# Performance work log

Measured on AMD Instinct MI355X. Metric: run time of the kernel, lower is better.

Reference implementation:

```python
import jax, jax.numpy as jnp
import numpy as np

EMBED_DIM = 1024
NUM_HEADS = 16
HEAD_DIM = EMBED_DIM // NUM_HEADS
SEQ_LEN = 2048
BATCH = 2


def setup_inputs() -> dict:
    key = jax.random.key(0)
    ks = jax.random.split(key, 9)
    s = 1.0 / np.sqrt(EMBED_DIM)
    inputs = jax.random.normal(ks[0], (BATCH, SEQ_LEN, EMBED_DIM), dtype=jnp.float32)
    Wq = jax.random.uniform(ks[1], (EMBED_DIM, EMBED_DIM), jnp.float32, -s, s)
    bq = jax.random.uniform(ks[2], (EMBED_DIM,), jnp.float32, -s, s)
    Wk = jax.random.uniform(ks[3], (EMBED_DIM, EMBED_DIM), jnp.float32, -s, s)
    bk = jax.random.uniform(ks[4], (EMBED_DIM,), jnp.float32, -s, s)
    Wv = jax.random.uniform(ks[5], (EMBED_DIM, EMBED_DIM), jnp.float32, -s, s)
    bv = jax.random.uniform(ks[6], (EMBED_DIM,), jnp.float32, -s, s)
    Wo = jax.random.uniform(ks[7], (EMBED_DIM, EMBED_DIM), jnp.float32, -s, s)
    bo = jax.random.uniform(ks[8], (EMBED_DIM,), jnp.float32, -s, s)
    return {"inputs": inputs, "Wq": Wq, "bq": bq, "Wk": Wk, "bk": bk,
            "Wv": Wv, "bv": bv, "Wo": Wo, "bo": bo}


def reference(inputs, Wq, bq, Wk, bk, Wv, bv, Wo, bo):
    B, S, D = inputs.shape
    H, Hd = NUM_HEADS, HEAD_DIM

    def heads(x):  # [B,S,D] -> [B,H,S,Hd]
        return x.reshape(B, S, H, Hd).transpose(0, 2, 1, 3)

    q = heads(inputs @ Wq + bq)
    k = heads(inputs @ Wk + bk)
    v = heads(inputs @ Wv + bv)

    # [B,H,S,S] causal scores (naive, matching original module)
    scores = jnp.einsum('bhqd,bhkd->bhqk', q, k) * (Hd ** -0.5)
    causal = jnp.tril(jnp.ones((S, S), dtype=bool))
    scores = jnp.where(causal, scores, jnp.float32(-jnp.inf))
    attn = jax.nn.softmax(scores, axis=-1)

    out = jnp.einsum('bhqk,bhkd->bhqd', attn, v)
    out = out.transpose(0, 2, 1, 3).reshape(B, S, D)
    return out @ Wo + bo
```

## Files before the change

kernel.cpp:

```cpp
#include <hip/hip_runtime.h>
#include <stdint.h>
#include <stddef.h>

#define SEQ   2048
#define DIM   1024
#define NH    16
#define HD    64
#define MTOT  4096
#define LPAD  72
#define EPAD  136
#define FPAD  132
#define QSCALE 0.18033688f

typedef __attribute__((ext_vector_type(8))) short short8;
typedef __attribute__((ext_vector_type(4))) float floatx4;
typedef __attribute__((ext_vector_type(16))) float floatx16;
typedef __attribute__((ext_vector_type(4))) float float4v;
typedef __attribute__((ext_vector_type(4))) unsigned short ushort4v;
typedef __attribute__((ext_vector_type(4))) unsigned int uint4v;

__device__ __forceinline__ floatx4 mfma_bf16(short8 a, short8 b, floatx4 c) {
    return __builtin_amdgcn_mfma_f32_16x16x32_bf16(a, b, c, 0, 0, 0);
}
__device__ __forceinline__ floatx16 mfma32(short8 a, short8 b, floatx16 c) {
    return __builtin_amdgcn_mfma_f32_32x32x16_bf16(a, b, c, 0, 0, 0);
}

__device__ __forceinline__ float b2f(unsigned short s) {
    unsigned int u = ((unsigned int)s) << 16;
    return __builtin_bit_cast(float, u);
}
__device__ __forceinline__ unsigned short f2b(float f) {
    unsigned int u = __builtin_bit_cast(unsigned int, f);
    u += 0x7fffu + ((u >> 16) & 1u);
    return (unsigned short)(u >> 16);
}
__device__ __forceinline__ unsigned int cvtpk(float lo, float hi) {
    unsigned int w;
    asm("v_cvt_pk_bf16_f32 %0, %1, %2" : "=v"(w) : "v"(lo), "v"(hi));
    return w;
}
__device__ __forceinline__ void swap32(unsigned int& a, unsigned int& b) {
    asm("v_permlane32_swap_b32 %0, %1" : "+v"(a), "+v"(b));
}
__device__ __forceinline__ float exp2v(float x) {
    float r;
    asm("v_exp_f32 %0, %1" : "=v"(r) : "v"(x));
    return r;
}
__device__ __forceinline__ short8 mk8(unsigned int a, unsigned int b,
                                      unsigned int c, unsigned int d) {
    uint4v u; u.x = a; u.y = b; u.z = c; u.w = d;
    return __builtin_bit_cast(short8, u);
}
__device__ __forceinline__ void g2l16(const unsigned short* g, unsigned short* l) {
    __builtin_amdgcn_global_load_lds(
        (const __attribute__((address_space(1))) void*)g,
        (__attribute__((address_space(3))) void*)l, 16, 0, 0);
}

__global__ __launch_bounds__(256) void prep_all(const float* __restrict__ w0,
                                                const float* __restrict__ w1,
                                                const float* __restrict__ w2,
                                                const float* __restrict__ w3,
                                                unsigned short* __restrict__ outbase,
                                                const float* __restrict__ xin,
                                                unsigned short* __restrict__ xout) {
    const int z = blockIdx.z;
    const int tid = threadIdx.x;
    if (z >= 4) {
        const int cblk = (z - 4) * 256 + blockIdx.y * 16 + blockIdx.x;
        const int i = (cblk * 256 + tid) * 4;
        const float4v v = *(const float4v*)&xin[i];
        ushort4v o;
        o.x = f2b(v.x); o.y = f2b(v.y); o.z = f2b(v.z); o.w = f2b(v.w);
        *(ushort4v*)&xout[i] = o;
        return;
    }
    __shared__ float t[64][65];
    const float* in = (z == 0) ? w0 : (z == 1) ? w1 : (z == 2) ? w2 : w3;
    unsigned short* out = outbase + (size_t)z * DIM * DIM;
    const int c0 = blockIdx.x * 64, r0 = blockIdx.y * 64;
    const int x = tid & 63, y = tid >> 6;
#pragma unroll
    for (int i = 0; i < 64; i += 4)
        t[y + i][x] = in[(size_t)(r0 + y + i) * DIM + c0 + x];
    __syncthreads();
#pragma unroll
    for (int i = 0; i < 64; i += 4)
        out[(size_t)(c0 + y + i) * DIM + r0 + x] = f2b(t[x][y + i]);
}

__global__ __launch_bounds__(256) void gemm_fused(const unsigned short* __restrict__ A,
                                                  const unsigned short* __restrict__ WTbase,
                                                  const float* __restrict__ b0,
                                                  const float* __restrict__ b1,
                                                  const float* __restrict__ b2,
                                                  void* __restrict__ outbase,
                                                  int qkv) {
    __shared__ __attribute__((aligned(16))) unsigned short smem[2 * 128 * LPAD];
    unsigned short* As = smem;
    unsigned short* Bs = smem + 128 * 64;

    const int z = blockIdx.z;
    const unsigned short* BT = WTbase + (size_t)z * (DIM * DIM);
    const float* bias        = (z == 0) ? b0 : (z == 1) ? b1 : b2;
    const int mode = qkv ? ((z == 0) ? 1 : (z == 1) ? 3 : 4) : 0;
    float* Cf          = (float*)outbase;
    unsigned short* Cb = (unsigned short*)outbase + (size_t)z * ((size_t)MTOT * DIM);

    const int tid = threadIdx.x;
    const int w = tid >> 6, lane = tid & 63;
    const int quad = lane >> 4, l16 = lane & 15;
    const int wm = w >> 1, wn = w & 1;
    const int m0 = blockIdx.x * 128, n0 = blockIdx.y * 128;
    const int bb = m0 >> 11;

    floatx4 acc[4][4];
#pragma unroll
    for (int mi = 0; mi < 4; ++mi)
#pragma unroll
        for (int ni = 0; ni < 4; ++ni) acc[mi][ni] = (floatx4)0.0f;

    const int srow8 = lane >> 3;
    const int sgs8  = ((lane & 7) ^ srow8) * 8;
    const unsigned short* gA = &A [(size_t)(m0 + w * 8 + srow8) * DIM + sgs8];
    const unsigned short* gB = &BT[(size_t)(n0 + w * 8 + srow8) * DIM + sgs8];

    const int sx = l16 & 7;

    for (int k0 = 0; ; k0 += 64) {
#pragma unroll
        for (int i = 0; i < 4; ++i) {
            g2l16(gA + (size_t)i * (32 * DIM) + k0, &As[(i * 4 + w) * 512]);
            g2l16(gB + (size_t)i * (32 * DIM) + k0, &Bs[(i * 4 + w) * 512]);
        }
        __syncthreads();
#pragma unroll
        for (int kk = 0; kk < 2; ++kk) {
            short8 a[4], b[4];
#pragma unroll
            for (int mi = 0; mi < 4; ++mi)
                a[mi] = *(const short8*)&As[(wm * 64 + mi * 16 + l16) * 64 +
                                            (((kk * 4) + quad) ^ sx) * 8];
#pragma unroll
            for (int ni = 0; ni < 4; ++ni)
                b[ni] = *(const short8*)&Bs[(wn * 64 + ni * 16 + l16) * 64 +
                                            (((kk * 4) + quad) ^ sx) * 8];
#pragma unroll
            for (int mi = 0; mi < 4; ++mi)
#pragma unroll
                for (int ni = 0; ni < 4; ++ni)
                    acc[mi][ni] = mfma_bf16(a[mi], b[ni], acc[mi][ni]);
        }
        if (k0 + 64 >= DIM) break;
        __syncthreads();
    }

    float bvv[4];
#pragma unroll
    for (int ni = 0; ni < 4; ++ni) bvv[ni] = bias[n0 + wn * 64 + ni * 16 + l16];

    if (mode == 0) {
        float* T = (float*)smem;
        for (int p = 0; p < 4; ++p) {
            __syncthreads();
            if (wm == (p >> 1)) {
                const int mib = (p & 1) * 2;
#pragma unroll
                for (int mm = 0; mm < 2; ++mm)
#pragma unroll
                    for (int ni = 0; ni < 4; ++ni)
#pragma unroll
                        for (int r = 0; r < 4; ++r)
                            T[(mm * 16 + quad * 4 + r) * FPAD + wn * 64 + ni * 16 + l16] =
                                acc[mib + mm][ni][r] + bvv[ni];
            }
            __syncthreads();
#pragma unroll
            for (int it = 0; it < 4; ++it) {
                const int c = it * 256 + tid;
                const int row = c >> 5, nof = (c & 31) * 4;
                *(float4v*)&Cf[(size_t)(m0 + p * 32 + row) * DIM + n0 + nof] =
                    *(const float4v*)&T[row * FPAD + nof];
            }
        }
    } else if (mode == 1) {
        unsigned short* T = smem;
        __syncthreads();
#pragma unroll
        for (int mi = 0; mi < 4; ++mi)
#pragma unroll
            for (int ni = 0; ni < 4; ++ni)
#pragma unroll
                for (int r = 0; r < 4; ++r)
                    T[(wm * 64 + mi * 16 + quad * 4 + r) * EPAD + wn * 64 + ni * 16 + l16] =
                        f2b((acc[mi][ni][r] + bvv[ni]) * QSCALE);
        __syncthreads();
#pragma unroll
        for (int it = 0; it < 8; ++it) {
            const int c = it * 256 + tid;
            const int seg = c >> 3, d8 = (c & 7) * 8;
            const int mm = seg >> 1, hseg = seg & 1;
            const int h = (n0 >> 6) + hseg;
            const int s = (m0 & (SEQ - 1)) + mm;
            *(short8*)&Cb[((size_t)(bb * NH + h) * SEQ + s) * HD + d8] =
                *(const short8*)&T[mm * EPAD + hseg * 64 + d8];
        }
    } else if (mode == 3) {
        unsigned short* T = smem;
        __syncthreads();
#pragma unroll
        for (int mi = 0; mi < 4; ++mi)
#pragma unroll
            for (int ni = 0; ni < 4; ++ni)
#pragma unroll
                for (int r = 0; r < 4; ++r)
                    T[(wm * 64 + mi * 16 + quad * 4 + r) * EPAD + wn * 64 + ni * 16 + l16] =
                        f2b(acc[mi][ni][r] + bvv[ni]);
        __syncthreads();
#pragma unroll
        for (int it = 0; it < 8; ++it) {
            const int f = it * 256 + tid;
            const int ln = f & 63, fragid = f >> 6;
            const int h2 = fragid >> 4;
            const int jb = (fragid >> 2) & 3;
            const int c  = fragid & 3;
            const short8 v = *(const short8*)&T[(jb * 32 + (ln & 31)) * EPAD +
                                                h2 * 64 + c * 16 + (ln >> 5) * 8];
            const int bh = bb * NH + (n0 >> 6) + h2;
            const int jg = ((m0 & (SEQ - 1)) >> 5) + jb;
            *(short8*)&Cb[(((size_t)bh * 64 + jg) * 4 + c) * 512 + ln * 8] = v;
        }
    } else {
        unsigned short* T = smem;
        __syncthreads();
#pragma unroll
        for (int mi = 0; mi < 4; ++mi)
#pragma unroll
            for (int ni = 0; ni < 4; ++ni) {
                ushort4v pk;
#pragma unroll
                for (int r = 0; r < 4; ++r) pk[r] = f2b(acc[mi][ni][r] + bvv[ni]);
                *(ushort4v*)&T[(wn * 64 + ni * 16 + l16) * EPAD + wm * 64 + mi * 16 + quad * 4] = pk;
            }
        __syncthreads();
#pragma unroll
        for (int it = 0; it < 8; ++it) {
            const int f = it * 256 + tid;
            const int ln = f & 63, fragid = f >> 6;
            const int h2 = fragid >> 4;
            const int jb = (fragid >> 2) & 3;
            const int dk = fragid & 3;
            const int d0 = dk >> 1, kk = dk & 1;
            const short8 v = *(const short8*)&T[(h2 * 64 + d0 * 32 + (ln & 31)) * EPAD +
                                                jb * 32 + kk * 16 + (ln >> 5) * 8];
            const int bh = bb * NH + (n0 >> 6) + h2;
            const int jg = ((m0 & (SEQ - 1)) >> 5) + jb;
            *(short8*)&Cb[(((size_t)bh * 64 + jg) * 4 + dk) * 512 + ln * 8] = v;
        }
    }
}

__global__ __launch_bounds__(256) void attn_fwd(const unsigned short* __restrict__ Q,
                                                const unsigned short* __restrict__ KP,
                                                const unsigned short* __restrict__ VP,
                                                unsigned short* __restrict__ O) {
    __shared__ float Fo[4][32][68];
    __shared__ float Fl[4][32];

    const int bh = blockIdx.x;
    const int pr = blockIdx.y;
    const int tid = threadIdx.x;
    const int w = tid >> 6, lane = tid & 63;
    const int ql  = lane & 31;
    const int hi  = lane >> 5;
    const int hi4 = hi * 4;
    const int hi8 = hi * 8;

    const unsigned short* Qh  = Q  + (size_t)bh * SEQ * HD;
    const unsigned short* KPh = KP + (size_t)bh * (64 * 2048);
    const unsigned short* VPh = VP + (size_t)bh * (64 * 2048);
    const int bb = bh >> 4, h = bh & 15;

#define LOADKV(KF, VF) do {                                                  \
        _Pragma("unroll")                                                    \
        for (int c_ = 0; c_ < 4; ++c_) {                                     \
            KF[c_] = *(const short8*)(kp + c_ * 512);                        \
            VF[c_] = *(const short8*)(vp + c_ * 512);                        \
        }                                                                    \
        kp += 4 * 2048; vp += 4 * 2048;                                      \
    } while (0)

#define ATT_BLOCK(KF, VF, MASKED) do {                                       \
        floatx16 st_ = (floatx16)0.0f;                                       \
        __builtin_amdgcn_s_setprio(1);                                       \
        _Pragma("unroll")                                                    \
        for (int c_ = 0; c_ < 4; ++c_) st_ = mfma32(KF[c_], qf[c_], st_);    \
        __builtin_amdgcn_s_setprio(0);                                       \
        float p_[16];                                                        \
        _Pragma("unroll")                                                    \
        for (int r_ = 0; r_ < 16; ++r_) {                                    \
            float e_ = exp2v(st_[r_]);                                       \
            if (MASKED)                                                      \
                e_ = (((r_ & 3) + 8 * (r_ >> 2) + hi4) > ql) ? 0.0f : e_;    \
            p_[r_] = e_;                                                     \
        }                                                                    \
        l0 += (p_[0] + p_[1]) + (p_[2] + p_[3]);                             \
        l1 += (p_[4] + p_[5]) + (p_[6] + p_[7]);                             \
        l0 += (p_[8] + p_[9]) + (p_[10] + p_[11]);                           \
        l1 += (p_[12] + p_[13]) + (p_[14] + p_[15]);                         \
        unsigned int w0_ = cvtpk(p_[0], p_[1]),   w2_ = cvtpk(p_[4], p_[5]); \
        unsigned int w1_ = cvtpk(p_[2], p_[3]),   w3_ = cvtpk(p_[6], p_[7]); \
        unsigned int w4_ = cvtpk(p_[8], p_[9]),   w6_ = cvtpk(p_[12], p_[13]); \
        unsigned int w5_ = cvtpk(p_[10], p_[11]), w7_ = cvtpk(p_[14], p_[15]); \
        swap32(w0_, w2_); swap32(w1_, w3_);                                  \
        swap32(w4_, w6_); swap32(w5_, w7_);                                  \
        const short8 pa0_ = mk8(w0_, w1_, w2_, w3_);                         \
        const short8 pa1_ = mk8(w4_, w5_, w6_, w7_);                         \
        __builtin_amdgcn_s_setprio(1);                                       \
        o_acc0 = mfma32(pa0_, VF[0], o_acc0);                                \
        o_acc1 = mfma32(pa0_, VF[2], o_acc1);                                \
        o_acc0 = mfma32(pa1_, VF[1], o_acc0);                                \
        o_acc1 = mfma32(pa1_, VF[3], o_acc1);                                \
        __builtin_amdgcn_s_setprio(0);                                       \
    } while (0)

#pragma unroll 1
    for (int t = 0; t < 2; ++t) {
        const int qc = t ? pr : (63 - pr);
        const int q0 = qc * 32;

        short8 qf[4];
#pragma unroll
        for (int c = 0; c < 4; ++c)
            qf[c] = *(const short8*)(Qh + (size_t)(q0 + ql) * HD + c * 16 + hi8);

        floatx16 o_acc0 = (floatx16)0.0f, o_acc1 = (floatx16)0.0f;
        float l0 = 0.0f, l1 = 0.0f;

        const int n = (qc >= w) ? ((qc - w) >> 2) + 1 : 0;
        const bool lastmask = ((qc & 3) == w);
        const unsigned short* kp = KPh + (size_t)w * 2048 + lane * 8;
        const unsigned short* vp = VPh + (size_t)w * 2048 + lane * 8;

        if (n > 0) {
            short8 kfA[4], vfA[4], kfB[4], vfB[4];
            LOADKV(kfA, vfA);
            int b = 0;
            while (b + 2 <= n - 1) {
                LOADKV(kfB, vfB);
                ATT_BLOCK(kfA, vfA, 0);
                LOADKV(kfA, vfA);
                ATT_BLOCK(kfB, vfB, 0);
                b += 2;
            }
            if (b == n - 2) {
                LOADKV(kfB, vfB);
                ATT_BLOCK(kfA, vfA, 0);
                ATT_BLOCK(kfB, vfB, lastmask);
            } else {
                ATT_BLOCK(kfA, vfA, lastmask);
            }
        }

        float* Fow = &Fo[w][0][0];
#pragma unroll
        for (int r = 0; r < 16; ++r) {
            const int row = (r & 3) + 8 * (r >> 2) + hi4;
            Fow[row * 68 + ql]      = o_acc0[r];
            Fow[row * 68 + 32 + ql] = o_acc1[r];
        }
        float l = l0 + l1;
        l += __shfl_xor(l, 32, 64);
        if (lane < 32) Fl[w][lane] = l;
        __syncthreads();

        const int rrow = w * 8 + (lane >> 3);
        const int c8   = (lane & 7) * 8;
        float s[8];
#pragma unroll
        for (int e = 0; e < 8; ++e) s[e] = 0.0f;
#pragma unroll
        for (int ww = 0; ww < 4; ++ww) {
            const float* src = &Fo[ww][rrow][c8];
            const float4v a = *(const float4v*)&src[0];
            const float4v b2 = *(const float4v*)&src[4];
            s[0] += a.x;  s[1] += a.y;  s[2] += a.z;  s[3] += a.w;
            s[4] += b2.x; s[5] += b2.y; s[6] += b2.z; s[7] += b2.w;
        }
        const float lt = (Fl[0][rrow] + Fl[1][rrow]) + (Fl[2][rrow] + Fl[3][rrow]);
        const float iv = 1.0f / lt;
        const unsigned int o0 = cvtpk(s[0] * iv, s[1] * iv);
        const unsigned int o1 = cvtpk(s[2] * iv, s[3] * iv);
        const unsigned int o2 = cvtpk(s[4] * iv, s[5] * iv);
        const unsigned int o3 = cvtpk(s[6] * iv, s[7] * iv);
        *(short8*)&O[(size_t)(bb * SEQ + q0 + rrow) * DIM + h * HD + c8] =
            mk8(o0, o1, o2, o3);
        __syncthreads();
    }
#undef LOADKV
#undef ATT_BLOCK
}

extern "C" void kernel_launch(void* const* d_in, const int* in_sizes, int n_in,
                              void* d_out, int out_size, void* d_ws, size_t ws_size,
                              hipStream_t stream) {
    const float* X  = (const float*)d_in[0];
    const float* Wq = (const float*)d_in[1];
    const float* bq = (const float*)d_in[2];
    const float* Wk = (const float*)d_in[3];
    const float* bk = (const float*)d_in[4];
    const float* Wv = (const float*)d_in[5];
    const float* bv = (const float*)d_in[6];
    const float* Wo = (const float*)d_in[7];
    const float* bo = (const float*)d_in[8];

    unsigned short* ws = (unsigned short*)d_ws;
    const size_t WSZ = (size_t)DIM * DIM;
    const size_t TSZ = (size_t)MTOT * DIM;
    unsigned short* WqT = ws;
    unsigned short* WoT = ws + 3 * WSZ;
    unsigned short* Qb  = ws + 4 * WSZ;
    unsigned short* Kp  = Qb + TSZ;
    unsigned short* Vp  = Kp + TSZ;
    unsigned short* Ob  = Vp + TSZ;

    unsigned short* Xb = (unsigned short*)d_out;

    prep_all<<<dim3(16, 16, 20), 256, 0, stream>>>(Wq, Wk, Wv, Wo, WqT, X, Xb);

    gemm_fused<<<dim3(MTOT / 128, DIM / 128, 3), 256, 0, stream>>>(
        Xb, WqT, bq, bk, bv, (void*)Qb, 1);

    attn_fwd<<<dim3(2 * NH, 32), 256, 0, stream>>>(Qb, Kp, Vp, Ob);

    gemm_fused<<<dim3(MTOT / 128, DIM / 128, 1), 256, 0, stream>>>(
        Ob, WoT, bo, bo, bo, d_out, 0);
}
```

Baseline: 171.9 us.

## Use single-wave attention blocks per query tile instead of 4-wave KV split

The attention kernel now launches one 64-thread wave per 32-row query tile, and that wave walks the whole causal KV range itself. Previously four waves split the KV blocks and reduced partial outputs through shared memory, and each block handled two paired query tiles for load balance. This drops the cross-wave float reduction and its barriers, and launches more, smaller blocks ordered heaviest-first. In exchange, each wave has a longer serial dependency chain, and balance now relies on the hardware scheduler. The row-sum accumulation was also moved after the PV MFMAs to overlap with them.

```diff
diff --git a/kernel.cpp b/kernel.cpp
--- a/kernel.cpp
+++ b/kernel.cpp
@@ -262,17 +262,16 @@
     }
 }
 
-__global__ __launch_bounds__(256) void attn_fwd(const unsigned short* __restrict__ Q,
-                                                const unsigned short* __restrict__ KP,
-                                                const unsigned short* __restrict__ VP,
-                                                unsigned short* __restrict__ O) {
-    __shared__ float Fo[4][32][68];
-    __shared__ float Fl[4][32];
+__global__ __launch_bounds__(64) void attn_fwd(const unsigned short* __restrict__ Q,
+                                               const unsigned short* __restrict__ KP,
+                                               const unsigned short* __restrict__ VP,
+                                               unsigned short* __restrict__ O) {
+    __shared__ __attribute__((aligned(16))) unsigned short Os[32 * LPAD];
+    __shared__ float Linv[32];
 
     const int bh = blockIdx.x;
-    const int pr = blockIdx.y;
-    const int tid = threadIdx.x;
-    const int w = tid >> 6, lane = tid & 63;
+    const int qc = (gridDim.y - 1) - blockIdx.y;
+    const int lane = threadIdx.x;
     const int ql  = lane & 31;
     const int hi  = lane >> 5;
     const int hi4 = hi * 4;
@@ -281,7 +280,18 @@
     const unsigned short* Qh  = Q  + (size_t)bh * SEQ * HD;
     const unsigned short* KPh = KP + (size_t)bh * (64 * 2048);
     const unsigned short* VPh = VP + (size_t)bh * (64 * 2048);
-    const int bb = bh >> 4, h = bh & 15;
+    const int q0 = qc * 32;
+
+    short8 qf[4];
+#pragma unroll
+    for (int c = 0; c < 4; ++c)
+        qf[c] = *(const short8*)(Qh + (size_t)(q0 + ql) * HD + c * 16 + hi8);
+
+    floatx16 o_acc0 = (floatx16)0.0f, o_acc1 = (floatx16)0.0f;
+    float l0 = 0.0f, l1 = 0.0f;
+
+    const unsigned short* kp = KPh + lane * 8;
+    const unsigned short* vp = VPh + lane * 8;
 
 #define LOADKV(KF, VF) do {                                                  \
         _Pragma("unroll")                                                    \
@@ -289,7 +299,7 @@
             KF[c_] = *(const short8*)(kp + c_ * 512);                        \
             VF[c_] = *(const short8*)(vp + c_ * 512);                        \
         }                                                                    \
-        kp += 4 * 2048; vp += 4 * 2048;                                      \
+        kp += 2048; vp += 2048;                                              \
     } while (0)
 
 #define ATT_BLOCK(KF, VF, MASKED) do {                                       \
@@ -306,10 +316,6 @@
                 e_ = (((r_ & 3) + 8 * (r_ >> 2) + hi4) > ql) ? 0.0f : e_;    \
             p_[r_] = e_;                                                     \
         }                                                                    \
-        l0 += (p_[0] + p_[1]) + (p_[2] + p_[3]);                             \
-        l1 += (p_[4] + p_[5]) + (p_[6] + p_[7]);                             \
-        l0 += (p_[8] + p_[9]) + (p_[10] + p_[11]);                           \
-        l1 += (p_[12] + p_[13]) + (p_[14] + p_[15]);                         \
         unsigned int w0_ = cvtpk(p_[0], p_[1]),   w2_ = cvtpk(p_[4], p_[5]); \
         unsigned int w1_ = cvtpk(p_[2], p_[3]),   w3_ = cvtpk(p_[6], p_[7]); \
         unsigned int w4_ = cvtpk(p_[8], p_[9]),   w6_ = cvtpk(p_[12], p_[13]); \
@@ -324,80 +330,50 @@
         o_acc0 = mfma32(pa1_, VF[1], o_acc0);                                \
         o_acc1 = mfma32(pa1_, VF[3], o_acc1);                                \
         __builtin_amdgcn_s_setprio(0);                                       \
+        l0 += (p_[0] + p_[1]) + (p_[2] + p_[3]);                             \
+        l1 += (p_[4] + p_[5]) + (p_[6] + p_[7]);                             \
+        l0 += (p_[8] + p_[9]) + (p_[10] + p_[11]);                           \
+        l1 += (p_[12] + p_[13]) + (p_[14] + p_[15]);                         \
     } while (0)
 
-#pragma unroll 1
-    for (int t = 0; t < 2; ++t) {
-        const int qc = t ? pr : (63 - pr);
-        const int q0 = qc * 32;
-
-        short8 qf[4];
-#pragma unroll
-        for (int c = 0; c < 4; ++c)
-            qf[c] = *(const short8*)(Qh + (size_t)(q0 + ql) * HD + c * 16 + hi8);
-
-        floatx16 o_acc0 = (floatx16)0.0f, o_acc1 = (floatx16)0.0f;
-        float l0 = 0.0f, l1 = 0.0f;
-
-        const int n = (qc >= w) ? ((qc - w) >> 2) + 1 : 0;
-        const bool lastmask = ((qc & 3) == w);
-        const unsigned short* kp = KPh + (size_t)w * 2048 + lane * 8;
-        const unsigned short* vp = VPh + (size_t)w * 2048 + lane * 8;
-
-        if (n > 0) {
-            short8 kfA[4], vfA[4], kfB[4], vfB[4];
-            LOADKV(kfA, vfA);
-            int b = 0;
-            while (b + 2 <= n - 1) {
-                LOADKV(kfB, vfB);
-                ATT_BLOCK(kfA, vfA, 0);
-                LOADKV(kfA, vfA);
-                ATT_BLOCK(kfB, vfB, 0);
-                b += 2;
-            }
-            if (b == n - 2) {
-                LOADKV(kfB, vfB);
-                ATT_BLOCK(kfA, vfA, 0);
-                ATT_BLOCK(kfB, vfB, lastmask);
-            } else {
-                ATT_BLOCK(kfA, vfA, lastmask);
-            }
-        }
-
-        float* Fow = &Fo[w][0][0];
-#pragma unroll
-        for (int r = 0; r < 16; ++r) {
-            const int row = (r & 3) + 8 * (r >> 2) + hi4;
-            Fow[row * 68 + ql]      = o_acc0[r];
-            Fow[row * 68 + 32 + ql] = o_acc1[r];
-        }
-        float l = l0 + l1;
-        l += __shfl_xor(l, 32, 64);
-        if (lane < 32) Fl[w][lane] = l;
-        __syncthreads();
-
-        const int rrow = w * 8 + (lane >> 3);
-        const int c8   = (lane & 7) * 8;
-        float s[8];
-#pragma unroll
-        for (int e = 0; e < 8; ++e) s[e] = 0.0f;
-#pragma unroll
-        for (int ww = 0; ww < 4; ++ww) {
-            const float* src = &Fo[ww][rrow][c8];
-            const float4v a = *(const float4v*)&src[0];
-            const float4v b2 = *(const float4v*)&src[4];
-            s[0] += a.x;  s[1] += a.y;  s[2] += a.z;  s[3] += a.w;
-            s[4] += b2.x; s[5] += b2.y; s[6] += b2.z; s[7] += b2.w;
-        }
-        const float lt = (Fl[0][rrow] + Fl[1][rrow]) + (Fl[2][rrow] + Fl[3][rrow]);
-        const float iv = 1.0f / lt;
-        const unsigned int o0 = cvtpk(s[0] * iv, s[1] * iv);
-        const unsigned int o1 = cvtpk(s[2] * iv, s[3] * iv);
-        const unsigned int o2 = cvtpk(s[4] * iv, s[5] * iv);
-        const unsigned int o3 = cvtpk(s[6] * iv, s[7] * iv);
-        *(short8*)&O[(size_t)(bb * SEQ + q0 + rrow) * DIM + h * HD + c8] =
-            mk8(o0, o1, o2, o3);
-        __syncthreads();
+    const int n = qc + 1;
+    short8 kfA[4], vfA[4], kfB[4], vfB[4];
+    LOADKV(kfA, vfA);
+    int b = 0;
+    while (b + 2 <= n - 1) {
+        LOADKV(kfB, vfB);
+        ATT_BLOCK(kfA, vfA, 0);
+        LOADKV(kfA, vfA);
+        ATT_BLOCK(kfB, vfB, 0);
+        b += 2;
+    }
+    if (b == n - 2) {
+        LOADKV(kfB, vfB);
+        ATT_BLOCK(kfA, vfA, 0);
+        ATT_BLOCK(kfB, vfB, 1);
+    } else {
+        ATT_BLOCK(kfA, vfA, 1);
+    }
+
+    float l = l0 + l1;
+    l += __shfl_xor(l, 32, 64);
+    const float inv = 1.0f / l;
+    if (lane < 32) Linv[lane] = inv;
+    __syncthreads();
+#pragma unroll
+    for (int r = 0; r < 16; ++r) {
+        const int row = (r & 3) + 8 * (r >> 2) + hi4;
+        const float iv = Linv[row];
+        Os[row * LPAD + ql]      = f2b(o_acc0[r] * iv);
+        Os[row * LPAD + 32 + ql] = f2b(o_acc1[r] * iv);
+    }
+    __syncthreads();
+    const int bb = bh >> 4, h = bh & 15;
+#pragma unroll
+    for (int it = 0; it < 4; ++it) {
+        const int row = it * 8 + (lane >> 3), d8 = (lane & 7) * 8;
+        *(short8*)&O[(size_t)(bb * SEQ + q0 + row) * DIM + h * HD + d8] =
+            *(const short8*)&Os[row * LPAD + d8];
     }
 #undef LOADKV
 #undef ATT_BLOCK
@@ -433,7 +409,7 @@
     gemm_fused<<<dim3(MTOT / 128, DIM / 128, 3), 256, 0, stream>>>(
         Xb, WqT, bq, bk, bv, (void*)Qb, 1);
 
-    attn_fwd<<<dim3(2 * NH, 32), 256, 0, stream>>>(Qb, Kp, Vp, Ob);
+    attn_fwd<<<dim3(2 * NH, SEQ / 32), 64, 0, stream>>>(Qb, Kp, Vp, Ob);
 
     gemm_fused<<<dim3(MTOT / 128, DIM / 128, 1), 256, 0, stream>>>(
         Ob, WoT, bo, bo, bo, d_out, 0);
```

After: 172.9 us. No clear change (+0.6%).
